# Optimization experiments

Measured on AMD Instinct MI355X. Metric: run time of the kernel, lower is better.

## Reference

```python
import jax, jax.numpy as jnp
import numpy as np

N = 100001      # item_num + 1
D = 64          # hidden_units
NNZ = 3200000   # number of nonzeros in encoder_adj (avg degree ~32)


def setup_inputs() -> dict:
    key = jax.random.key(0)
    k1, k2, k3, k4 = jax.random.split(key, 4)
    row_idx = jax.random.randint(k1, (NNZ,), 0, N, dtype=jnp.int32)
    col_idx = jax.random.randint(k2, (NNZ,), 0, N, dtype=jnp.int32)
    adj_vals = jax.random.uniform(k3, (NNZ,), dtype=jnp.float32)
    emb_weight = jax.random.normal(k4, (N, D), dtype=jnp.float32)
    return {"row_idx": row_idx, "col_idx": col_idx, "adj_vals": adj_vals,
            "emb_weight": emb_weight}


def _spmm(row_idx, col_idx, vals, x):
    # COO SpMM: out[r] += vals[e] * x[col[e]]  -> [N, D]
    gathered = vals[:, None] * x[col_idx]          # [NNZ, D]
    return jax.ops.segment_sum(gathered, row_idx, num_segments=N)


def reference(row_idx, col_idx, adj_vals, emb_weight):
    e0 = emb_weight                                 # ego embeddings
    e1 = _spmm(row_idx, col_idx, adj_vals, e0)      # GCN layer 1
    e2 = _spmm(row_idx, col_idx, adj_vals, e1)      # GCN layer 2
    summed = e0 + e1 + e2                           # sum(embeds)
    return (summed, e0, e1, e2)
```

## Files before the change

### kernel.cpp

```cpp
#include <hip/hip_runtime.h>
#include <stdint.h>

#define DHID 64
#define G_BLOCKS 256
#define BMAX 512

static inline size_t align256(size_t x) { return (x + 255) & ~(size_t)255; }


__global__ void zero_i32(int* __restrict__ p, int n) {
  int i = blockIdx.x * blockDim.x + threadIdx.x;
  if (i < n) p[i] = 0;
}

__global__ void zero_f32(float* __restrict__ p, size_t n) {
  size_t i = (size_t)blockIdx.x * blockDim.x + threadIdx.x;
  if (i < n) p[i] = 0.f;
}


__global__ void a1_hist_k(const int* __restrict__ row, int* __restrict__ histGB,
                          int nnz, int B, int chunk) {
  __shared__ int h[BMAX];
  for (int i = threadIdx.x; i < B; i += blockDim.x) h[i] = 0;
  __syncthreads();
  int g = blockIdx.x;
  int s = g * chunk, e = min(nnz, s + chunk);
  for (int j = s + threadIdx.x; j < e; j += blockDim.x)
    atomicAdd(&h[row[j] >> 8], 1);
  __syncthreads();
  for (int i = threadIdx.x; i < B; i += blockDim.x)
    histGB[i * G_BLOCKS + g] = h[i];
}

__global__ void scan_gb_k(const int* __restrict__ histGB, int* __restrict__ offGB,
                          int* __restrict__ btot, int B) {
  __shared__ int wsum[4];
  int b = blockIdx.x, t = threadIdx.x, lane = t & 63, w = t >> 6;
  int v = histGB[b * G_BLOCKS + t];
  int incl = v;
#pragma unroll
  for (int off = 1; off < 64; off <<= 1) {
    int u = __shfl_up(incl, off);
    if (lane >= off) incl += u;
  }
  if (lane == 63) wsum[w] = incl;
  __syncthreads();
  int woff = 0;
  for (int w2 = 0; w2 < w; ++w2) woff += wsum[w2];
  offGB[b * G_BLOCKS + t] = woff + incl - v;
  if (t == 0) btot[b] = wsum[0] + wsum[1] + wsum[2] + wsum[3];
}

__global__ void scan_b_k(const int* __restrict__ btot, int* __restrict__ base, int B) {
  __shared__ int wsum[4];
  int t = threadIdx.x, lane = t & 63, w = t >> 6;
  int i0 = 2 * t, i1 = 2 * t + 1;
  int v0 = (i0 < B) ? btot[i0] : 0;
  int v1 = (i1 < B) ? btot[i1] : 0;
  int ps = v0 + v1, incl = ps;
#pragma unroll
  for (int off = 1; off < 64; off <<= 1) {
    int u = __shfl_up(incl, off);
    if (lane >= off) incl += u;
  }
  if (lane == 63) wsum[w] = incl;
  __syncthreads();
  int woff = 0;
  for (int w2 = 0; w2 < w; ++w2) woff += wsum[w2];
  int ex = woff + incl - ps;
  if (i0 <= B) base[i0] = ex;
  if (i1 <= B) base[i1] = ex + v0;
}

__global__ void a2_scatter_k(const int* __restrict__ row, const int* __restrict__ col,
                             const float* __restrict__ val, const int* __restrict__ base,
                             const int* __restrict__ offGB, int2* __restrict__ stage,
                             int nnz, int B, int chunk) {
  __shared__ int cur[BMAX];
  int g = blockIdx.x;
  for (int i = threadIdx.x; i < B; i += blockDim.x)
    cur[i] = base[i] + offGB[i * G_BLOCKS + g];
  __syncthreads();
  int s = g * chunk, e = min(nnz, s + chunk);
  for (int j = s + threadIdx.x; j < e; j += blockDim.x) {
    int r = row[j];
    int b = r >> 8;
    int pos = atomicAdd(&cur[b], 1);
    int2 p;
    p.x = ((r & 255) << 24) | col[j];
    p.y = __float_as_int(val[j]);
    stage[pos] = p;
  }
}


__global__ void b1_hist_k(const int2* __restrict__ stage, const int* __restrict__ base,
                          int* __restrict__ count, int n) {
  __shared__ int h[256];
  int b = blockIdx.x, t = threadIdx.x;
  h[t] = 0;
  __syncthreads();
  int s = base[b], e = base[b + 1];
  for (int j = s + t; j < e; j += 256)
    atomicAdd(&h[((unsigned)stage[j].x) >> 24], 1);
  __syncthreads();
  int r = (b << 8) + t;
  if (r < n) count[r] = h[t];
}

__global__ void b2_scatter_k(const int2* __restrict__ stage, const int* __restrict__ base,
                             const int* __restrict__ rowstart, int2* __restrict__ edges,
                             int n) {
  __shared__ int cur[256];
  int b = blockIdx.x, t = threadIdx.x;
  int r = (b << 8) + t;
  cur[t] = (r < n) ? rowstart[r] : 0;
  __syncthreads();
  int s = base[b], e = base[b + 1];
  for (int j = s + t; j < e; j += 256) {
    int2 p = stage[j];
    int rlow = ((unsigned)p.x) >> 24;
    int pos = atomicAdd(&cur[rlow], 1);
    int2 q;
    q.x = p.x & 0xFFFFFF;
    q.y = p.y;
    edges[pos] = q;
  }
}


__global__ void scan1_k(const int* __restrict__ count, int* __restrict__ bsum, int n) {
  __shared__ int lds[4];
  int base = blockIdx.x * 2048 + threadIdx.x * 8;
  int s = 0;
#pragma unroll
  for (int i = 0; i < 8; ++i) { int idx = base + i; if (idx < n) s += count[idx]; }
#pragma unroll
  for (int off = 32; off > 0; off >>= 1) s += __shfl_down(s, off);
  if ((threadIdx.x & 63) == 0) lds[threadIdx.x >> 6] = s;
  __syncthreads();
  if (threadIdx.x == 0) bsum[blockIdx.x] = lds[0] + lds[1] + lds[2] + lds[3];
}

__global__ void scan2_k(int* __restrict__ bsum, int nb, int* __restrict__ rowstart, int n) {
  int lane = threadIdx.x;
  int v = (lane < nb) ? bsum[lane] : 0;
  int incl = v;
#pragma unroll
  for (int off = 1; off < 64; off <<= 1) {
    int t = __shfl_up(incl, off);
    if (lane >= off) incl += t;
  }
  if (lane < nb) bsum[lane] = incl - v;
  if (lane == 63) rowstart[n] = incl;
}

__global__ void scan3_k(const int* __restrict__ count, const int* __restrict__ bsum,
                        int* __restrict__ rowstart, int n) {
  __shared__ int wsum[4];
  int base = blockIdx.x * 2048 + threadIdx.x * 8;
  int vals[8];
  int s = 0;
#pragma unroll
  for (int i = 0; i < 8; ++i) { int idx = base + i; vals[i] = (idx < n) ? count[idx] : 0; s += vals[i]; }
  int lane = threadIdx.x & 63, wid = threadIdx.x >> 6;
  int incl = s;
#pragma unroll
  for (int off = 1; off < 64; off <<= 1) {
    int t = __shfl_up(incl, off);
    if (lane >= off) incl += t;
  }
  if (lane == 63) wsum[wid] = incl;
  __syncthreads();
  int run = bsum[blockIdx.x] + (incl - s);
  for (int w = 0; w < wid; ++w) run += wsum[w];
#pragma unroll
  for (int i = 0; i < 8; ++i) {
    int idx = base + i;
    if (idx < n) rowstart[idx] = run;
    run += vals[i];
  }
}


__global__ void spmm_k(const int* __restrict__ rowstart, const int2* __restrict__ edges,
                       const float* __restrict__ x, float* __restrict__ y, int n) {
  int wave = (blockIdx.x * blockDim.x + threadIdx.x) >> 6;
  int lane = threadIdx.x & 63;
  if (wave >= n) return;
  int start = __builtin_amdgcn_readfirstlane(rowstart[wave]);
  int end   = __builtin_amdgcn_readfirstlane(rowstart[wave + 1]);
  float acc = 0.f;
  int k = start;
  for (; k + 8 <= end; k += 8) {
    int2 e0 = edges[k + 0], e1 = edges[k + 1], e2 = edges[k + 2], e3 = edges[k + 3];
    int2 e4 = edges[k + 4], e5 = edges[k + 5], e6 = edges[k + 6], e7 = edges[k + 7];
    float x0 = x[((size_t)e0.x << 6) + lane];
    float x1 = x[((size_t)e1.x << 6) + lane];
    float x2 = x[((size_t)e2.x << 6) + lane];
    float x3 = x[((size_t)e3.x << 6) + lane];
    float x4 = x[((size_t)e4.x << 6) + lane];
    float x5 = x[((size_t)e5.x << 6) + lane];
    float x6 = x[((size_t)e6.x << 6) + lane];
    float x7 = x[((size_t)e7.x << 6) + lane];
    acc += __int_as_float(e0.y) * x0;
    acc += __int_as_float(e1.y) * x1;
    acc += __int_as_float(e2.y) * x2;
    acc += __int_as_float(e3.y) * x3;
    acc += __int_as_float(e4.y) * x4;
    acc += __int_as_float(e5.y) * x5;
    acc += __int_as_float(e6.y) * x6;
    acc += __int_as_float(e7.y) * x7;
  }
  for (; k < end; ++k) {
    int2 e = edges[k];
    acc += __int_as_float(e.y) * x[((size_t)e.x << 6) + lane];
  }
  y[((size_t)wave << 6) + lane] = acc;
}

__global__ void spmm_fused_k(const int* __restrict__ rowstart, const int2* __restrict__ edges,
                             const float* __restrict__ e0, const float* __restrict__ e1,
                             float* __restrict__ e2, float* __restrict__ summed,
                             float* __restrict__ e0out, int n) {
  int wave = (blockIdx.x * blockDim.x + threadIdx.x) >> 6;
  int lane = threadIdx.x & 63;
  if (wave >= n) return;
  int start = __builtin_amdgcn_readfirstlane(rowstart[wave]);
  int end   = __builtin_amdgcn_readfirstlane(rowstart[wave + 1]);
  float acc = 0.f;
  int k = start;
  for (; k + 8 <= end; k += 8) {
    int2 ea = edges[k + 0], eb = edges[k + 1], ec = edges[k + 2], ed = edges[k + 3];
    int2 ee = edges[k + 4], ef = edges[k + 5], eg = edges[k + 6], eh = edges[k + 7];
    float x0 = e1[((size_t)ea.x << 6) + lane];
    float x1 = e1[((size_t)eb.x << 6) + lane];
    float x2 = e1[((size_t)ec.x << 6) + lane];
    float x3 = e1[((size_t)ed.x << 6) + lane];
    float x4 = e1[((size_t)ee.x << 6) + lane];
    float x5 = e1[((size_t)ef.x << 6) + lane];
    float x6 = e1[((size_t)eg.x << 6) + lane];
    float x7 = e1[((size_t)eh.x << 6) + lane];
    acc += __int_as_float(ea.y) * x0;
    acc += __int_as_float(eb.y) * x1;
    acc += __int_as_float(ec.y) * x2;
    acc += __int_as_float(ed.y) * x3;
    acc += __int_as_float(ee.y) * x4;
    acc += __int_as_float(ef.y) * x5;
    acc += __int_as_float(eg.y) * x6;
    acc += __int_as_float(eh.y) * x7;
  }
  for (; k < end; ++k) {
    int2 e = edges[k];
    acc += __int_as_float(e.y) * e1[((size_t)e.x << 6) + lane];
  }
  size_t o = ((size_t)wave << 6) + lane;
  float v0 = e0[o];
  float v1 = e1[o];
  e2[o] = acc;
  summed[o] = v0 + v1 + acc;
  e0out[o] = v0;
}


__global__ void spmm_atomic_k(const int* __restrict__ row, const int* __restrict__ col,
                              const float* __restrict__ val, const float* __restrict__ x,
                              float* __restrict__ y, int nnz) {
  int wave = (blockIdx.x * blockDim.x + threadIdx.x) >> 6;
  int lane = threadIdx.x & 63;
  if (wave >= nnz) return;
  int r = row[wave]; int c = col[wave]; float v = val[wave];
  atomicAdd(&y[(size_t)r * DHID + lane], v * x[(size_t)c * DHID + lane]);
}

__global__ void sum_k(const float4* __restrict__ e0, const float4* __restrict__ e1,
                      const float4* __restrict__ e2, float4* __restrict__ summed,
                      float4* __restrict__ e0out, int n4) {
  int i = blockIdx.x * blockDim.x + threadIdx.x;
  if (i < n4) {
    float4 a = e0[i], b = e1[i], c = e2[i];
    float4 s;
    s.x = a.x + b.x + c.x;
    s.y = a.y + b.y + c.y;
    s.z = a.z + b.z + c.z;
    s.w = a.w + b.w + c.w;
    summed[i] = s;
    e0out[i] = a;
  }
}

extern "C" void kernel_launch(void* const* d_in, const int* in_sizes, int n_in,
                              void* d_out, int out_size, void* d_ws, size_t ws_size,
                              hipStream_t stream) {
  const int*   row = (const int*)d_in[0];
  const int*   col = (const int*)d_in[1];
  const float* val = (const float*)d_in[2];
  const float* emb = (const float*)d_in[3];
  int nnz = in_sizes[0];
  int n   = in_sizes[3] / DHID;
  size_t ND = (size_t)n * DHID;

  float* out    = (float*)d_out;
  float* summed = out;
  float* e0o    = out + ND;
  float* e1     = out + 2 * ND;
  float* e2     = out + 3 * ND;

  int B  = (n + 255) >> 8;
  int nb = (n + 2047) / 2048;
  int chunk = (nnz + G_BLOCKS - 1) / G_BLOCKS;

  size_t o0 = 0;
  size_t count_off    = o0; o0 += align256((size_t)(n + 1) * 4);
  size_t rowstart_off = o0; o0 += align256((size_t)(n + 1) * 4);
  size_t bsum_off     = o0; o0 += align256(256 * 4);
  size_t histGB_off   = o0; o0 += align256((size_t)BMAX * G_BLOCKS * 4);
  size_t offGB_off    = o0; o0 += align256((size_t)BMAX * G_BLOCKS * 4);
  size_t btot_off     = o0; o0 += align256((size_t)BMAX * 4);
  size_t base_off     = o0; o0 += align256((size_t)(BMAX + 1) * 4);
  size_t stage_off    = o0; o0 += align256((size_t)nnz * 8);
  size_t edges_off    = o0; o0 += align256((size_t)nnz * 8);
  size_t need_sorted = o0;

  bool use_sorted = (ws_size >= need_sorted) && (B <= BMAX) && (nb <= 64) &&
                    (n < (1 << 24));

  int rb = (int)((ND + 255) / 256);
  int n4 = (int)(ND / 4);
  int sb = (n4 + 255) / 256;
  int wb = (int)(((size_t)nnz * 64 + 255) / 256);

  if (use_sorted) {
    uint8_t* w = (uint8_t*)d_ws;
    int*  count    = (int*)(w + count_off);
    int*  rowstart = (int*)(w + rowstart_off);
    int*  bsum     = (int*)(w + bsum_off);
    int*  histGB   = (int*)(w + histGB_off);
    int*  offGB    = (int*)(w + offGB_off);
    int*  btot     = (int*)(w + btot_off);
    int*  base     = (int*)(w + base_off);
    int2* stage    = (int2*)(w + stage_off);
    int2* edges    = (int2*)(w + edges_off);

    a1_hist_k<<<G_BLOCKS, 256, 0, stream>>>(row, histGB, nnz, B, chunk);
    scan_gb_k<<<B, 256, 0, stream>>>(histGB, offGB, btot, B);
    scan_b_k<<<1, 256, 0, stream>>>(btot, base, B);
    a2_scatter_k<<<G_BLOCKS, 256, 0, stream>>>(row, col, val, base, offGB, stage,
                                               nnz, B, chunk);
    b1_hist_k<<<B, 256, 0, stream>>>(stage, base, count, n);
    scan1_k<<<nb, 256, 0, stream>>>(count, bsum, n);
    scan2_k<<<1, 64, 0, stream>>>(bsum, nb, rowstart, n);
    scan3_k<<<nb, 256, 0, stream>>>(count, bsum, rowstart, n);
    b2_scatter_k<<<B, 256, 0, stream>>>(stage, base, rowstart, edges, n);

    spmm_k<<<rb, 256, 0, stream>>>(rowstart, edges, emb, e1, n);
    spmm_fused_k<<<rb, 256, 0, stream>>>(rowstart, edges, emb, e1, e2, summed, e0o, n);
  } else {
    zero_f32<<<(int)((ND + 255) / 256), 256, 0, stream>>>(e1, ND);
    spmm_atomic_k<<<wb, 256, 0, stream>>>(row, col, val, emb, e1, nnz);
    zero_f32<<<(int)((ND + 255) / 256), 256, 0, stream>>>(e2, ND);
    spmm_atomic_k<<<wb, 256, 0, stream>>>(row, col, val, e1, e2, nnz);
    sum_k<<<sb, 256, 0, stream>>>((const float4*)emb, (const float4*)e1,
                                  (const float4*)e2, (float4*)summed,
                                  (float4*)e0o, n4);
  }
}
```

Before: 485.5 us.

## Replace two-pass bucketed COO-to-CSR sort with direct global-atomic histogram and scatter

```diff
diff --git a/kernel.cpp b/kernel.cpp
--- a/kernel.cpp
+++ b/kernel.cpp
@@ -2,8 +2,6 @@
 #include <stdint.h>
 
 #define DHID 64
-#define G_BLOCKS 256
-#define BMAX 512
 
 static inline size_t align256(size_t x) { return (x + 255) & ~(size_t)255; }
 
@@ -19,116 +17,12 @@
 }
 
 
-__global__ void a1_hist_k(const int* __restrict__ row, int* __restrict__ histGB,
-                          int nnz, int B, int chunk) {
-  __shared__ int h[BMAX];
-  for (int i = threadIdx.x; i < B; i += blockDim.x) h[i] = 0;
-  __syncthreads();
-  int g = blockIdx.x;
-  int s = g * chunk, e = min(nnz, s + chunk);
-  for (int j = s + threadIdx.x; j < e; j += blockDim.x)
-    atomicAdd(&h[row[j] >> 8], 1);
-  __syncthreads();
-  for (int i = threadIdx.x; i < B; i += blockDim.x)
-    histGB[i * G_BLOCKS + g] = h[i];
-}
-
-__global__ void scan_gb_k(const int* __restrict__ histGB, int* __restrict__ offGB,
-                          int* __restrict__ btot, int B) {
-  __shared__ int wsum[4];
-  int b = blockIdx.x, t = threadIdx.x, lane = t & 63, w = t >> 6;
-  int v = histGB[b * G_BLOCKS + t];
-  int incl = v;
-#pragma unroll
-  for (int off = 1; off < 64; off <<= 1) {
-    int u = __shfl_up(incl, off);
-    if (lane >= off) incl += u;
-  }
-  if (lane == 63) wsum[w] = incl;
-  __syncthreads();
-  int woff = 0;
-  for (int w2 = 0; w2 < w; ++w2) woff += wsum[w2];
-  offGB[b * G_BLOCKS + t] = woff + incl - v;
-  if (t == 0) btot[b] = wsum[0] + wsum[1] + wsum[2] + wsum[3];
-}
-
-__global__ void scan_b_k(const int* __restrict__ btot, int* __restrict__ base, int B) {
-  __shared__ int wsum[4];
-  int t = threadIdx.x, lane = t & 63, w = t >> 6;
-  int i0 = 2 * t, i1 = 2 * t + 1;
-  int v0 = (i0 < B) ? btot[i0] : 0;
-  int v1 = (i1 < B) ? btot[i1] : 0;
-  int ps = v0 + v1, incl = ps;
-#pragma unroll
-  for (int off = 1; off < 64; off <<= 1) {
-    int u = __shfl_up(incl, off);
-    if (lane >= off) incl += u;
-  }
-  if (lane == 63) wsum[w] = incl;
-  __syncthreads();
-  int woff = 0;
-  for (int w2 = 0; w2 < w; ++w2) woff += wsum[w2];
-  int ex = woff + incl - ps;
-  if (i0 <= B) base[i0] = ex;
-  if (i1 <= B) base[i1] = ex + v0;
-}
-
-__global__ void a2_scatter_k(const int* __restrict__ row, const int* __restrict__ col,
-                             const float* __restrict__ val, const int* __restrict__ base,
-                             const int* __restrict__ offGB, int2* __restrict__ stage,
-                             int nnz, int B, int chunk) {
-  __shared__ int cur[BMAX];
-  int g = blockIdx.x;
-  for (int i = threadIdx.x; i < B; i += blockDim.x)
-    cur[i] = base[i] + offGB[i * G_BLOCKS + g];
-  __syncthreads();
-  int s = g * chunk, e = min(nnz, s + chunk);
-  for (int j = s + threadIdx.x; j < e; j += blockDim.x) {
-    int r = row[j];
-    int b = r >> 8;
-    int pos = atomicAdd(&cur[b], 1);
-    int2 p;
-    p.x = ((r & 255) << 24) | col[j];
-    p.y = __float_as_int(val[j]);
-    stage[pos] = p;
-  }
-}
-
-
-__global__ void b1_hist_k(const int2* __restrict__ stage, const int* __restrict__ base,
-                          int* __restrict__ count, int n) {
-  __shared__ int h[256];
-  int b = blockIdx.x, t = threadIdx.x;
-  h[t] = 0;
-  __syncthreads();
-  int s = base[b], e = base[b + 1];
-  for (int j = s + t; j < e; j += 256)
-    atomicAdd(&h[((unsigned)stage[j].x) >> 24], 1);
-  __syncthreads();
-  int r = (b << 8) + t;
-  if (r < n) count[r] = h[t];
-}
-
-__global__ void b2_scatter_k(const int2* __restrict__ stage, const int* __restrict__ base,
-                             const int* __restrict__ rowstart, int2* __restrict__ edges,
-                             int n) {
-  __shared__ int cur[256];
-  int b = blockIdx.x, t = threadIdx.x;
-  int r = (b << 8) + t;
-  cur[t] = (r < n) ? rowstart[r] : 0;
-  __syncthreads();
-  int s = base[b], e = base[b + 1];
-  for (int j = s + t; j < e; j += 256) {
-    int2 p = stage[j];
-    int rlow = ((unsigned)p.x) >> 24;
-    int pos = atomicAdd(&cur[rlow], 1);
-    int2 q;
-    q.x = p.x & 0xFFFFFF;
-    q.y = p.y;
-    edges[pos] = q;
-  }
-}
-
+__global__ void hist_k(const int* __restrict__ row, int* __restrict__ count, int nnz) {
+  int i = blockIdx.x * blockDim.x + threadIdx.x;
+  int stride = gridDim.x * blockDim.x;
+  for (int j = i; j < nnz; j += stride)
+    atomicAdd(&count[row[j]], 1);
+}
 
 __global__ void scan1_k(const int* __restrict__ count, int* __restrict__ bsum, int n) {
   __shared__ int lds[4];
@@ -157,7 +51,7 @@
 }
 
 __global__ void scan3_k(const int* __restrict__ count, const int* __restrict__ bsum,
-                        int* __restrict__ rowstart, int n) {
+                        int* __restrict__ rowstart, int* __restrict__ cursor, int n) {
   __shared__ int wsum[4];
   int base = blockIdx.x * 2048 + threadIdx.x * 8;
   int vals[8];
@@ -178,8 +72,23 @@
 #pragma unroll
   for (int i = 0; i < 8; ++i) {
     int idx = base + i;
-    if (idx < n) rowstart[idx] = run;
+    if (idx < n) { rowstart[idx] = run; cursor[idx] = run; }
     run += vals[i];
+  }
+}
+
+__global__ void scatter_k(const int* __restrict__ row, const int* __restrict__ col,
+                          const float* __restrict__ val, int* __restrict__ cursor,
+                          int2* __restrict__ edges, int nnz) {
+  int i = blockIdx.x * blockDim.x + threadIdx.x;
+  int stride = gridDim.x * blockDim.x;
+  for (int j = i; j < nnz; j += stride) {
+    int r = row[j];
+    int pos = atomicAdd(&cursor[r], 1);
+    int2 q;
+    q.x = col[j];
+    q.y = __float_as_int(val[j]);
+    edges[pos] = q;
   }
 }
 
@@ -307,24 +216,17 @@
   float* e1     = out + 2 * ND;
   float* e2     = out + 3 * ND;
 
-  int B  = (n + 255) >> 8;
   int nb = (n + 2047) / 2048;
-  int chunk = (nnz + G_BLOCKS - 1) / G_BLOCKS;
 
   size_t o0 = 0;
   size_t count_off    = o0; o0 += align256((size_t)(n + 1) * 4);
   size_t rowstart_off = o0; o0 += align256((size_t)(n + 1) * 4);
+  size_t cursor_off   = o0; o0 += align256((size_t)(n + 1) * 4);
   size_t bsum_off     = o0; o0 += align256(256 * 4);
-  size_t histGB_off   = o0; o0 += align256((size_t)BMAX * G_BLOCKS * 4);
-  size_t offGB_off    = o0; o0 += align256((size_t)BMAX * G_BLOCKS * 4);
-  size_t btot_off     = o0; o0 += align256((size_t)BMAX * 4);
-  size_t base_off     = o0; o0 += align256((size_t)(BMAX + 1) * 4);
-  size_t stage_off    = o0; o0 += align256((size_t)nnz * 8);
   size_t edges_off    = o0; o0 += align256((size_t)nnz * 8);
   size_t need_sorted = o0;
 
-  bool use_sorted = (ws_size >= need_sorted) && (B <= BMAX) && (nb <= 64) &&
-                    (n < (1 << 24));
+  bool use_sorted = (ws_size >= need_sorted) && (nb <= 64);
 
   int rb = (int)((ND + 255) / 256);
   int n4 = (int)(ND / 4);
@@ -335,24 +237,16 @@
     uint8_t* w = (uint8_t*)d_ws;
     int*  count    = (int*)(w + count_off);
     int*  rowstart = (int*)(w + rowstart_off);
+    int*  cursor   = (int*)(w + cursor_off);
     int*  bsum     = (int*)(w + bsum_off);
-    int*  histGB   = (int*)(w + histGB_off);
-    int*  offGB    = (int*)(w + offGB_off);
-    int*  btot     = (int*)(w + btot_off);
-    int*  base     = (int*)(w + base_off);
-    int2* stage    = (int2*)(w + stage_off);
     int2* edges    = (int2*)(w + edges_off);
 
-    a1_hist_k<<<G_BLOCKS, 256, 0, stream>>>(row, histGB, nnz, B, chunk);
-    scan_gb_k<<<B, 256, 0, stream>>>(histGB, offGB, btot, B);
-    scan_b_k<<<1, 256, 0, stream>>>(btot, base, B);
-    a2_scatter_k<<<G_BLOCKS, 256, 0, stream>>>(row, col, val, base, offGB, stage,
-                                               nnz, B, chunk);
-    b1_hist_k<<<B, 256, 0, stream>>>(stage, base, count, n);
+    zero_i32<<<(n + 255) / 256, 256, 0, stream>>>(count, n);
+    hist_k<<<2048, 256, 0, stream>>>(row, count, nnz);
     scan1_k<<<nb, 256, 0, stream>>>(count, bsum, n);
     scan2_k<<<1, 64, 0, stream>>>(bsum, nb, rowstart, n);
-    scan3_k<<<nb, 256, 0, stream>>>(count, bsum, rowstart, n);
-    b2_scatter_k<<<B, 256, 0, stream>>>(stage, base, rowstart, edges, n);
+    scan3_k<<<nb, 256, 0, stream>>>(count, bsum, rowstart, cursor, n);
+    scatter_k<<<2048, 256, 0, stream>>>(row, col, val, cursor, edges, nnz);
 
     spmm_k<<<rb, 256, 0, stream>>>(rowstart, edges, emb, e1, n);
     spmm_fused_k<<<rb, 256, 0, stream>>>(rowstart, edges, emb, e1, e2, summed, e0o, n);
```

After: 692.3 us. 42.6% more time.

## Fuse second-pass sort into one kernel with 64-row buckets and local scan

Applied to the files above, without the earlier changes.

```diff
diff --git a/kernel.cpp b/kernel.cpp
--- a/kernel.cpp
+++ b/kernel.cpp
@@ -3,15 +3,11 @@
 
 #define DHID 64
 #define G_BLOCKS 256
-#define BMAX 512
+#define BMAX 2048
+#define RPB 64
 
 static inline size_t align256(size_t x) { return (x + 255) & ~(size_t)255; }
 
-
-__global__ void zero_i32(int* __restrict__ p, int n) {
-  int i = blockIdx.x * blockDim.x + threadIdx.x;
-  if (i < n) p[i] = 0;
-}
 
 __global__ void zero_f32(float* __restrict__ p, size_t n) {
   size_t i = (size_t)blockIdx.x * blockDim.x + threadIdx.x;
@@ -27,7 +23,7 @@
   int g = blockIdx.x;
   int s = g * chunk, e = min(nnz, s + chunk);
   for (int j = s + threadIdx.x; j < e; j += blockDim.x)
-    atomicAdd(&h[row[j] >> 8], 1);
+    atomicAdd(&h[row[j] >> 6], 1);
   __syncthreads();
   for (int i = threadIdx.x; i < B; i += blockDim.x)
     histGB[i * G_BLOCKS + g] = h[i];
@@ -55,10 +51,15 @@
 __global__ void scan_b_k(const int* __restrict__ btot, int* __restrict__ base, int B) {
   __shared__ int wsum[4];
   int t = threadIdx.x, lane = t & 63, w = t >> 6;
-  int i0 = 2 * t, i1 = 2 * t + 1;
-  int v0 = (i0 < B) ? btot[i0] : 0;
-  int v1 = (i1 < B) ? btot[i1] : 0;
-  int ps = v0 + v1, incl = ps;
+  int v[8];
+  int s = 0;
+#pragma unroll
+  for (int i = 0; i < 8; ++i) {
+    int idx = t * 8 + i;
+    v[i] = (idx < B) ? btot[idx] : 0;
+    s += v[i];
+  }
+  int incl = s;
 #pragma unroll
   for (int off = 1; off < 64; off <<= 1) {
     int u = __shfl_up(incl, off);
@@ -66,11 +67,14 @@
   }
   if (lane == 63) wsum[w] = incl;
   __syncthreads();
-  int woff = 0;
-  for (int w2 = 0; w2 < w; ++w2) woff += wsum[w2];
-  int ex = woff + incl - ps;
-  if (i0 <= B) base[i0] = ex;
-  if (i1 <= B) base[i1] = ex + v0;
+  int run = incl - s;
+  for (int w2 = 0; w2 < w; ++w2) run += wsum[w2];
+#pragma unroll
+  for (int i = 0; i < 8; ++i) {
+    int idx = t * 8 + i;
+    if (idx <= B) base[idx] = run;
+    run += v[i];
+  }
 }
 
 __global__ void a2_scatter_k(const int* __restrict__ row, const int* __restrict__ col,
@@ -85,39 +89,43 @@
   int s = g * chunk, e = min(nnz, s + chunk);
   for (int j = s + threadIdx.x; j < e; j += blockDim.x) {
     int r = row[j];
-    int b = r >> 8;
+    int b = r >> 6;
     int pos = atomicAdd(&cur[b], 1);
     int2 p;
-    p.x = ((r & 255) << 24) | col[j];
+    p.x = ((r & 63) << 24) | col[j];
     p.y = __float_as_int(val[j]);
     stage[pos] = p;
   }
 }
 
 
-__global__ void b1_hist_k(const int2* __restrict__ stage, const int* __restrict__ base,
-                          int* __restrict__ count, int n) {
-  __shared__ int h[256];
+__global__ __launch_bounds__(256) void
+bgroup_k(const int* __restrict__ base, const int2* __restrict__ stage,
+         int2* __restrict__ edges, int* __restrict__ rowstart, int n, int nnz) {
+  __shared__ int h[RPB];
+  __shared__ int cur[RPB];
   int b = blockIdx.x, t = threadIdx.x;
-  h[t] = 0;
+  if (t < RPB) h[t] = 0;
   __syncthreads();
   int s = base[b], e = base[b + 1];
   for (int j = s + t; j < e; j += 256)
     atomicAdd(&h[((unsigned)stage[j].x) >> 24], 1);
   __syncthreads();
-  int r = (b << 8) + t;
-  if (r < n) count[r] = h[t];
-}
-
-__global__ void b2_scatter_k(const int2* __restrict__ stage, const int* __restrict__ base,
-                             const int* __restrict__ rowstart, int2* __restrict__ edges,
-                             int n) {
-  __shared__ int cur[256];
-  int b = blockIdx.x, t = threadIdx.x;
-  int r = (b << 8) + t;
-  cur[t] = (r < n) ? rowstart[r] : 0;
-  __syncthreads();
-  int s = base[b], e = base[b + 1];
+  if (t < RPB) {
+    int v = h[t];
+    int incl = v;
+#pragma unroll
+    for (int off = 1; off < 64; off <<= 1) {
+      int u = __shfl_up(incl, off);
+      if (t >= off) incl += u;
+    }
+    int excl = incl - v;
+    cur[t] = s + excl;
+    int r = (b << 6) + t;
+    if (r < n) rowstart[r] = s + excl;
+  }
+  if (b == 0 && t == 0) rowstart[n] = nnz;
+  __syncthreads();
   for (int j = s + t; j < e; j += 256) {
     int2 p = stage[j];
     int rlow = ((unsigned)p.x) >> 24;
@@ -126,60 +134,6 @@
     q.x = p.x & 0xFFFFFF;
     q.y = p.y;
     edges[pos] = q;
-  }
-}
-
-
-__global__ void scan1_k(const int* __restrict__ count, int* __restrict__ bsum, int n) {
-  __shared__ int lds[4];
-  int base = blockIdx.x * 2048 + threadIdx.x * 8;
-  int s = 0;
-#pragma unroll
-  for (int i = 0; i < 8; ++i) { int idx = base + i; if (idx < n) s += count[idx]; }
-#pragma unroll
-  for (int off = 32; off > 0; off >>= 1) s += __shfl_down(s, off);
-  if ((threadIdx.x & 63) == 0) lds[threadIdx.x >> 6] = s;
-  __syncthreads();
-  if (threadIdx.x == 0) bsum[blockIdx.x] = lds[0] + lds[1] + lds[2] + lds[3];
-}
-
-__global__ void scan2_k(int* __restrict__ bsum, int nb, int* __restrict__ rowstart, int n) {
-  int lane = threadIdx.x;
-  int v = (lane < nb) ? bsum[lane] : 0;
-  int incl = v;
-#pragma unroll
-  for (int off = 1; off < 64; off <<= 1) {
-    int t = __shfl_up(incl, off);
-    if (lane >= off) incl += t;
-  }
-  if (lane < nb) bsum[lane] = incl - v;
-  if (lane == 63) rowstart[n] = incl;
-}
-
-__global__ void scan3_k(const int* __restrict__ count, const int* __restrict__ bsum,
-                        int* __restrict__ rowstart, int n) {
-  __shared__ int wsum[4];
-  int base = blockIdx.x * 2048 + threadIdx.x * 8;
-  int vals[8];
-  int s = 0;
-#pragma unroll
-  for (int i = 0; i < 8; ++i) { int idx = base + i; vals[i] = (idx < n) ? count[idx] : 0; s += vals[i]; }
-  int lane = threadIdx.x & 63, wid = threadIdx.x >> 6;
-  int incl = s;
-#pragma unroll
-  for (int off = 1; off < 64; off <<= 1) {
-    int t = __shfl_up(incl, off);
-    if (lane >= off) incl += t;
-  }
-  if (lane == 63) wsum[wid] = incl;
-  __syncthreads();
-  int run = bsum[blockIdx.x] + (incl - s);
-  for (int w = 0; w < wid; ++w) run += wsum[w];
-#pragma unroll
-  for (int i = 0; i < 8; ++i) {
-    int idx = base + i;
-    if (idx < n) rowstart[idx] = run;
-    run += vals[i];
   }
 }
 
@@ -307,24 +261,20 @@
   float* e1     = out + 2 * ND;
   float* e2     = out + 3 * ND;
 
-  int B  = (n + 255) >> 8;
-  int nb = (n + 2047) / 2048;
+  int B  = (n + RPB - 1) / RPB;
   int chunk = (nnz + G_BLOCKS - 1) / G_BLOCKS;
 
   size_t o0 = 0;
-  size_t count_off    = o0; o0 += align256((size_t)(n + 1) * 4);
-  size_t rowstart_off = o0; o0 += align256((size_t)(n + 1) * 4);
-  size_t bsum_off     = o0; o0 += align256(256 * 4);
   size_t histGB_off   = o0; o0 += align256((size_t)BMAX * G_BLOCKS * 4);
   size_t offGB_off    = o0; o0 += align256((size_t)BMAX * G_BLOCKS * 4);
   size_t btot_off     = o0; o0 += align256((size_t)BMAX * 4);
   size_t base_off     = o0; o0 += align256((size_t)(BMAX + 1) * 4);
+  size_t rowstart_off = o0; o0 += align256((size_t)(n + 1) * 4);
   size_t stage_off    = o0; o0 += align256((size_t)nnz * 8);
   size_t edges_off    = o0; o0 += align256((size_t)nnz * 8);
   size_t need_sorted = o0;
 
-  bool use_sorted = (ws_size >= need_sorted) && (B <= BMAX) && (nb <= 64) &&
-                    (n < (1 << 24));
+  bool use_sorted = (ws_size >= need_sorted) && (B <= BMAX) && (n < (1 << 24));
 
   int rb = (int)((ND + 255) / 256);
   int n4 = (int)(ND / 4);
@@ -333,13 +283,11 @@
 
   if (use_sorted) {
     uint8_t* w = (uint8_t*)d_ws;
-    int*  count    = (int*)(w + count_off);
-    int*  rowstart = (int*)(w + rowstart_off);
-    int*  bsum     = (int*)(w + bsum_off);
     int*  histGB   = (int*)(w + histGB_off);
     int*  offGB    = (int*)(w + offGB_off);
     int*  btot     = (int*)(w + btot_off);
     int*  base     = (int*)(w + base_off);
+    int*  rowstart = (int*)(w + rowstart_off);
     int2* stage    = (int2*)(w + stage_off);
     int2* edges    = (int2*)(w + edges_off);
 
@@ -348,11 +296,7 @@
     scan_b_k<<<1, 256, 0, stream>>>(btot, base, B);
     a2_scatter_k<<<G_BLOCKS, 256, 0, stream>>>(row, col, val, base, offGB, stage,
                                                nnz, B, chunk);
-    b1_hist_k<<<B, 256, 0, stream>>>(stage, base, count, n);
-    scan1_k<<<nb, 256, 0, stream>>>(count, bsum, n);
-    scan2_k<<<1, 64, 0, stream>>>(bsum, nb, rowstart, n);
-    scan3_k<<<nb, 256, 0, stream>>>(count, bsum, rowstart, n);
-    b2_scatter_k<<<B, 256, 0, stream>>>(stage, base, rowstart, edges, n);
+    bgroup_k<<<B, 256, 0, stream>>>(base, stage, edges, rowstart, n, nnz);
 
     spmm_k<<<rb, 256, 0, stream>>>(rowstart, edges, emb, e1, n);
     spmm_fused_k<<<rb, 256, 0, stream>>>(rowstart, edges, emb, e1, e2, summed, e0o, n);
```

Measured after the change: 492.2 us. No clear change (+1.4%).
